# Optimization experiments

Measured on AMD Instinct MI355X. Metric: run time of the kernel, lower is better.

## Reference

```python
import jax, jax.numpy as jnp
import numpy as np

N_QUBITS = 10
DEPTH = 4
BATCH = 2048


def _ry(state, theta, q, n):
    # RY(theta) = [[cos(t/2), -sin(t/2)], [sin(t/2), cos(t/2)]], per-sample theta [B]
    B = state.shape[0]
    st = state.reshape(B, 2 ** q, 2, 2 ** (n - q - 1))
    c = jnp.cos(theta * 0.5)[:, None, None]
    s = jnp.sin(theta * 0.5)[:, None, None]
    a0, a1 = st[:, :, 0], st[:, :, 1]
    out = jnp.stack([c * a0 - s * a1, s * a0 + c * a1], axis=2)
    return out.reshape(B, -1)


def _rx(state, theta, q, n):
    # RX(theta) = [[cos(t/2), -i sin(t/2)], [-i sin(t/2), cos(t/2)]], shared scalar theta
    B = state.shape[0]
    st = state.reshape(B, 2 ** q, 2, 2 ** (n - q - 1))
    c = jnp.cos(theta * 0.5)
    s = jnp.sin(theta * 0.5)
    a0, a1 = st[:, :, 0], st[:, :, 1]
    out = jnp.stack([c * a0 - 1j * s * a1, -1j * s * a0 + c * a1], axis=2)
    return out.reshape(B, -1)


def _cnot(state, ctrl, tgt, n):
    # flip target amplitudes in the control=1 subspace
    B = state.shape[0]
    lo, hi = min(ctrl, tgt), max(ctrl, tgt)
    st = state.reshape(B, 2 ** lo, 2, 2 ** (hi - lo - 1), 2, 2 ** (n - hi - 1))
    if ctrl == lo:
        s0 = st[:, :, 0]                      # [B, 2^lo, mid, 2, rest]
        s1 = jnp.flip(st[:, :, 1], axis=3)    # flip target (axis 3 after indexing)
        out = jnp.stack([s0, s1], axis=2)
    else:
        s0 = st[:, :, :, :, 0]                # [B, 2^lo, 2, mid, rest]
        s1 = jnp.flip(st[:, :, :, :, 1], axis=2)  # flip target (axis 2)
        out = jnp.stack([s0, s1], axis=4)
    return out.reshape(B, -1)


def _circuit(x, w):
    B, n = x.shape
    depth = w.shape[0]
    state = jnp.zeros((B, 2 ** n), dtype=jnp.complex64).at[:, 0].set(1.0)
    # AngleEmbedding with RY rotations, per-sample angles
    for q in range(n):
        state = _ry(state, x[:, q], q, n)
    # BasicEntanglerLayers: RX on every wire, then CNOT ring
    for l in range(depth):
        for q in range(n):
            state = _rx(state, w[l, q], q, n)
        if n == 2:
            state = _cnot(state, 0, 1, n)
        else:
            for q in range(n):
                state = _cnot(state, q, (q + 1) % n, n)
    probs = state.real ** 2 + state.imag ** 2  # [B, 2^n]
    zs = []
    for q in range(n):
        m = probs.reshape(B, 2 ** q, 2, -1).sum(axis=(1, 3))  # marginal over wire q
        zs.append(m[:, 0] - m[:, 1])
    return jnp.stack(zs, axis=1)  # [B, n]


def setup_inputs() -> dict:
    key = jax.random.key(0)
    kx, kw = jax.random.split(key)
    x = jax.random.normal(kx, (BATCH, N_QUBITS), dtype=jnp.float32)
    q_weights = 0.02 * jax.random.normal(kw, (DEPTH, N_QUBITS), dtype=jnp.float32)
    return {"x": x, "q_weights": q_weights}


def reference(x, q_weights):
    return _circuit(x, q_weights)
```

## Files before the change

kernel.cpp:

```cpp
#include <hip/hip_runtime.h>

#define NQ 10
#define NR 16


__device__ __forceinline__ float xf(int i) { return __int_as_float(i); }
__device__ __forceinline__ int   fx(float f) { return __float_as_int(f); }

template<int M>
__device__ __forceinline__ float lane_xor(float v, int a32) {
    if constexpr (M == 1)
        return xf(__builtin_amdgcn_update_dpp(fx(v), fx(v), 0xB1, 0xF, 0xF, true));
    else if constexpr (M == 2)
        return xf(__builtin_amdgcn_update_dpp(fx(v), fx(v), 0x4E, 0xF, 0xF, true));
    else if constexpr (M == 8)
        return xf(__builtin_amdgcn_update_dpp(fx(v), fx(v), 0x128, 0xF, 0xF, true));
    else if constexpr (M == 4)
        return xf(__builtin_amdgcn_ds_swizzle(fx(v), 0x101F));
    else if constexpr (M == 16)
        return xf(__builtin_amdgcn_ds_swizzle(fx(v), 0x401F));
    else
        return xf(__builtin_amdgcn_ds_bpermute(a32, fx(v)));
}

__global__ __launch_bounds__(256, 2) void vql_kernel(
    const float* __restrict__ x,
    const float* __restrict__ w,
    float* __restrict__ out)
{
    const int lane = threadIdx.x & 63;
    const int b = blockIdx.x * 4 + (threadIdx.x >> 6);
    const int a32 = (lane ^ 32) << 2;

    const float2* xr = reinterpret_cast<const float2*>(x + b * NQ);
    const float2 x01 = xr[0], x23 = xr[1], x45 = xr[2], x67 = xr[3], x89 = xr[4];
    const float xa[NQ] = {0.5f * x01.x, 0.5f * x01.y, 0.5f * x23.x, 0.5f * x23.y,
                          0.5f * x45.x, 0.5f * x45.y, 0.5f * x67.x, 0.5f * x67.y,
                          0.5f * x89.x, 0.5f * x89.y};

    float F0r[NQ], F0i[NQ], F1r[NQ], F1i[NQ];
    #pragma unroll
    for (int q = 0; q < NQ; ++q) {
        float sy, cy, s, c;
        __sincosf(xa[q], &sy, &cy);
        __sincosf(0.5f * w[q], &s, &c);
        const float v0r = c * cy,  v0i = -s * sy;
        const float v1r = c * sy,  v1i = -s * cy;
        F0r[q] = v0r + v1r;  F0i[q] = v0i + v1i;
        F1r[q] = v0r - v1r;  F1i[q] = v0i - v1i;
    }

    const int L0 = lane & 1,        L1 = (lane >> 1) & 1, L2 = (lane >> 2) & 1;
    const int L3 = (lane >> 3) & 1, L4 = (lane >> 4) & 1, L5 = (lane >> 5) & 1;
    const int PL1 = L0 ^ L1, PL2 = PL1 ^ L2, PL3 = PL2 ^ L3, PL4 = PL3 ^ L4;
    const int g[7] = {PL4, PL4 ^ L5, PL3 ^ L5, PL2 ^ L5, PL1 ^ L5, L0 ^ L5, L5};
    #define SR_(q,bit) ((bit) ? F1r[q] : F0r[q])
    #define SI_(q,bit) ((bit) ? F1i[q] : F0i[q])

    float A_r[2], A_i[2];
    #pragma unroll
    for (int t = 0; t < 2; ++t) {
        float ar = SR_(0, g[0] ^ t), ai = SI_(0, g[0] ^ t);
        #pragma unroll
        for (int q = 1; q < 7; ++q) {
            const float br = SR_(q, g[q] ^ t), bi = SI_(q, g[q] ^ t);
            const float nr = ar * br - ai * bi;
            const float ni = ar * bi + ai * br;
            ar = nr; ai = ni;
        }
        A_r[t] = ar * (1.0f / 1024.0f);
        A_i[t] = ai * (1.0f / 1024.0f);
    }
    float Gr[2][2], Gi[2][2];
    #pragma unroll
    for (int t2 = 0; t2 < 2; ++t2)
        #pragma unroll
        for (int t1 = 0; t1 < 2; ++t1) {
            const float ar = SR_(8, t2 ^ L5), ai = SI_(8, t2 ^ L5);
            const float br = SR_(9, t1 ^ L5), bi = SI_(9, t1 ^ L5);
            Gr[t2][t1] = ar * br - ai * bi;
            Gi[t2][t1] = ar * bi + ai * br;
        }
    float Br_[2][2][2], Bi_[2][2][2];
    #pragma unroll
    for (int t3 = 0; t3 < 2; ++t3)
        #pragma unroll
        for (int t2 = 0; t2 < 2; ++t2)
            #pragma unroll
            for (int t1 = 0; t1 < 2; ++t1) {
                const float ar = SR_(7, t3 ^ L5), ai = SI_(7, t3 ^ L5);
                Br_[t3][t2][t1] = ar * Gr[t2][t1] - ai * Gi[t2][t1];
                Bi_[t3][t2][t1] = ar * Gi[t2][t1] + ai * Gr[t2][t1];
            }
    float re[NR], im[NR];
    #pragma unroll
    for (int r = 0; r < NR; ++r) {
        const int r0 = r & 1, r1 = (r >> 1) & 1, r2 = (r >> 2) & 1, r3 = (r >> 3) & 1;
        const int p1 = r0, p2 = r0 ^ r1, p3 = p2 ^ r2, p4 = p3 ^ r3;
        const float br = Br_[p3][p2][p1], bi = Bi_[p3][p2][p1];
        re[r] = A_r[p4] * br - A_i[p4] * bi;
        im[r] = A_r[p4] * bi + A_i[p4] * br;
    }
    #undef SR_
    #undef SI_

    float h1[NQ], h2[NQ], h3[NQ];
    #pragma unroll
    for (int q = 0; q < NQ; ++q) {
        h1[q] = 0.5f * w[NQ + q];
        h2[q] = 0.5f * w[2 * NQ + q];
        h3[q] = 0.5f * w[3 * NQ + q];
    }
    #define SG_(M) ((__builtin_popcount(lane & (M)) & 1) ? -1.f : 1.f)
    const float s1 = SG_(1),  s2 = SG_(2),  s3 = SG_(3),  s4 = SG_(4),  s5 = SG_(5);
    const float s6 = SG_(6),  s8 = SG_(8),  s10 = SG_(10), s12 = SG_(12);
    const float s16 = SG_(16), s20 = SG_(20), s24 = SG_(24), s32 = SG_(32);
    const float s40 = SG_(40), s48 = SG_(48);
    #undef SG_

    float C[NR];
    C[0]  = s32 * h1[0] + s16 * h1[1] + s8 * h1[2] + s4 * h1[3] + s2 * h1[4] + s1 * h1[5]
          + s48 * h2[0] + s24 * h2[1] + s12 * h2[2] + s6 * h2[3] + s3 * h2[4]
          + s40 * h3[0] + s20 * h3[1] + s10 * h3[2] + s5 * h3[3];
    C[8]  = h1[6] + s1 * h2[5] + s2 * h3[4];
    C[4]  = h1[7] + s1 * h3[5];
    C[2]  = h1[8] + s48 * h3[8];
    C[1]  = h1[9] + s48 * h2[9] + s24 * h3[9];
    C[12] = h2[6];
    C[6]  = h2[7];
    C[3]  = h2[8];
    C[10] = h3[6];
    C[5]  = h3[7];
    C[7] = 0.f; C[9] = 0.f; C[11] = 0.f; C[13] = 0.f; C[14] = 0.f; C[15] = 0.f;

    #pragma unroll
    for (int bset = 0; bset < 4; ++bset) {
        const int bb = 1 << bset;
        #pragma unroll
        for (int r = 0; r < NR; ++r) {
            if (!(r & bb)) {
                const float u = C[r], v = C[r | bb];
                C[r] = u + v;  C[r | bb] = u - v;
            }
        }
    }
    #pragma unroll
    for (int r = 0; r < NR; ++r) {
        float sp, cp;
        __sincosf(C[r], &sp, &cp);
        const float nr = re[r] * cp + im[r] * sp;
        const float ni = im[r] * cp - re[r] * sp;
        re[r] = nr; im[r] = ni;
    }

    #pragma unroll
    for (int bset = 0; bset < 4; ++bset) {
        const int bb = 1 << bset;
        #pragma unroll
        for (int r = 0; r < NR; ++r) {
            if (!(r & bb)) {
                float u = re[r], v = re[r | bb];
                re[r] = u + v;  re[r | bb] = u - v;
                u = im[r]; v = im[r | bb];
                im[r] = u + v;  im[r | bb] = u - v;
            }
        }
    }
    {
        const float sgA = (lane &  1) ? -1.f : 1.f;
        const float sgB = (lane &  2) ? -1.f : 1.f;
        const float sgC = (lane &  4) ? -1.f : 1.f;
        const float sgD = (lane &  8) ? -1.f : 1.f;
        const float sgE = (lane & 16) ? -1.f : 1.f;
        const float sgF = (lane & 32) ? -1.f : 1.f;
        #pragma unroll
        for (int r = 0; r < NR; ++r) {
            float p;
            p = lane_xor< 1>(re[r], a32); re[r] = fmaf(sgA, re[r], p);
            p = lane_xor< 1>(im[r], a32); im[r] = fmaf(sgA, im[r], p);
            p = lane_xor< 2>(re[r], a32); re[r] = fmaf(sgB, re[r], p);
            p = lane_xor< 2>(im[r], a32); im[r] = fmaf(sgB, im[r], p);
            p = lane_xor< 4>(re[r], a32); re[r] = fmaf(sgC, re[r], p);
            p = lane_xor< 4>(im[r], a32); im[r] = fmaf(sgC, im[r], p);
            p = lane_xor< 8>(re[r], a32); re[r] = fmaf(sgD, re[r], p);
            p = lane_xor< 8>(im[r], a32); im[r] = fmaf(sgD, im[r], p);
            p = lane_xor<16>(re[r], a32); re[r] = fmaf(sgE, re[r], p);
            p = lane_xor<16>(im[r], a32); im[r] = fmaf(sgE, im[r], p);
            p = lane_xor<32>(re[r], a32); re[r] = fmaf(sgF, re[r], p);
            p = lane_xor<32>(im[r], a32); im[r] = fmaf(sgF, im[r], p);
        }
    }

    float W[NR];
    #pragma unroll
    for (int r = 0; r < NR; ++r) W[r] = re[r] * re[r] + im[r] * im[r];
    #pragma unroll
    for (int bset = 0; bset < 4; ++bset) {
        const int bb = 1 << bset;
        #pragma unroll
        for (int r = 0; r < NR; ++r) {
            if (!(r & bb)) {
                const float u = W[r], v = W[r | bb];
                W[r] = u + v;  W[r | bb] = u - v;
            }
        }
    }
    const float sg44 = (__builtin_popcount(lane & 44) & 1) ? -1.f : 1.f;
    const float sg26 = (__builtin_popcount(lane & 26) & 1) ? -1.f : 1.f;
    const float sg13 = (__builtin_popcount(lane & 13) & 1) ? -1.f : 1.f;
    const float sg38 = (__builtin_popcount(lane & 38) & 1) ? -1.f : 1.f;
    const float sg51 = (__builtin_popcount(lane & 51) & 1) ? -1.f : 1.f;
    const float sg25 = (__builtin_popcount(lane & 25) & 1) ? -1.f : 1.f;
    const float sg12 = (__builtin_popcount(lane & 12) & 1) ? -1.f : 1.f;

    float z[NQ];
    z[0] = sg44 * W[12];
    z[1] = sg26 * W[10];
    z[2] = sg13 * W[ 5];
    z[3] = sg38 * W[10];
    z[4] = sg51 * W[ 5];
    z[5] = sg25 * W[10];
    z[6] = sg12 * W[13];
    z[7] = sg38 * W[ 6];
    z[8] = sg51 * W[ 3];
    z[9] = sg25 * W[ 9];

    #pragma unroll
    for (int q = 0; q < NQ; ++q) {
        z[q] += lane_xor<1>(z[q], a32);
        z[q] += lane_xor<2>(z[q], a32);
        z[q] += lane_xor<4>(z[q], a32);
        z[q] += lane_xor<8>(z[q], a32);
        z[q] += lane_xor<16>(z[q], a32);
        z[q] += lane_xor<32>(z[q], a32);
    }
    if (lane == 0) {
        float2* op = reinterpret_cast<float2*>(out + b * NQ);
        op[0] = make_float2(z[0], z[1]);
        op[1] = make_float2(z[2], z[3]);
        op[2] = make_float2(z[4], z[5]);
        op[3] = make_float2(z[6], z[7]);
        op[4] = make_float2(z[8], z[9]);
    }
}

extern "C" void kernel_launch(void* const* d_in, const int* in_sizes, int n_in,
                              void* d_out, int out_size, void* d_ws, size_t ws_size,
                              hipStream_t stream) {
    const float* x = (const float*)d_in[0];
    const float* w = (const float*)d_in[1];
    float* out = (float*)d_out;
    const int B = in_sizes[0] / NQ;
    vql_kernel<<<B / 4, 256, 0, stream>>>(x, w, out);
}
```

Measured before the change: 11.05 us.

## Compute Z expectations via correlation with permuted Fourier state instead of inverse transform

```diff
diff --git a/kernel.cpp b/kernel.cpp
--- a/kernel.cpp
+++ b/kernel.cpp
@@ -68,8 +68,8 @@
             const float ni = ar * bi + ai * br;
             ar = nr; ai = ni;
         }
-        A_r[t] = ar * (1.0f / 1024.0f);
-        A_i[t] = ai * (1.0f / 1024.0f);
+        A_r[t] = ar * (1.0f / 32.0f);
+        A_i[t] = ai * (1.0f / 32.0f);
     }
     float Gr[2][2], Gi[2][2];
     #pragma unroll
@@ -153,77 +153,122 @@
         re[r] = nr; im[r] = ni;
     }
 
-    #pragma unroll
-    for (int bset = 0; bset < 4; ++bset) {
-        const int bb = 1 << bset;
-        #pragma unroll
-        for (int r = 0; r < NR; ++r) {
-            if (!(r & bb)) {
-                float u = re[r], v = re[r | bb];
-                re[r] = u + v;  re[r | bb] = u - v;
-                u = im[r]; v = im[r | bb];
-                im[r] = u + v;  im[r | bb] = u - v;
-            }
-        }
-    }
-    {
-        const float sgA = (lane &  1) ? -1.f : 1.f;
-        const float sgB = (lane &  2) ? -1.f : 1.f;
-        const float sgC = (lane &  4) ? -1.f : 1.f;
-        const float sgD = (lane &  8) ? -1.f : 1.f;
-        const float sgE = (lane & 16) ? -1.f : 1.f;
-        const float sgF = (lane & 32) ? -1.f : 1.f;
-        #pragma unroll
-        for (int r = 0; r < NR; ++r) {
-            float p;
-            p = lane_xor< 1>(re[r], a32); re[r] = fmaf(sgA, re[r], p);
-            p = lane_xor< 1>(im[r], a32); im[r] = fmaf(sgA, im[r], p);
-            p = lane_xor< 2>(re[r], a32); re[r] = fmaf(sgB, re[r], p);
-            p = lane_xor< 2>(im[r], a32); im[r] = fmaf(sgB, im[r], p);
-            p = lane_xor< 4>(re[r], a32); re[r] = fmaf(sgC, re[r], p);
-            p = lane_xor< 4>(im[r], a32); im[r] = fmaf(sgC, im[r], p);
-            p = lane_xor< 8>(re[r], a32); re[r] = fmaf(sgD, re[r], p);
-            p = lane_xor< 8>(im[r], a32); im[r] = fmaf(sgD, im[r], p);
-            p = lane_xor<16>(re[r], a32); re[r] = fmaf(sgE, re[r], p);
-            p = lane_xor<16>(im[r], a32); im[r] = fmaf(sgE, im[r], p);
-            p = lane_xor<32>(re[r], a32); re[r] = fmaf(sgF, re[r], p);
-            p = lane_xor<32>(im[r], a32); im[r] = fmaf(sgF, im[r], p);
-        }
-    }
-
-    float W[NR];
-    #pragma unroll
-    for (int r = 0; r < NR; ++r) W[r] = re[r] * re[r] + im[r] * im[r];
-    #pragma unroll
-    for (int bset = 0; bset < 4; ++bset) {
-        const int bb = 1 << bset;
-        #pragma unroll
-        for (int r = 0; r < NR; ++r) {
-            if (!(r & bb)) {
-                const float u = W[r], v = W[r | bb];
-                W[r] = u + v;  W[r | bb] = u - v;
-            }
-        }
-    }
-    const float sg44 = (__builtin_popcount(lane & 44) & 1) ? -1.f : 1.f;
-    const float sg26 = (__builtin_popcount(lane & 26) & 1) ? -1.f : 1.f;
-    const float sg13 = (__builtin_popcount(lane & 13) & 1) ? -1.f : 1.f;
-    const float sg38 = (__builtin_popcount(lane & 38) & 1) ? -1.f : 1.f;
-    const float sg51 = (__builtin_popcount(lane & 51) & 1) ? -1.f : 1.f;
-    const float sg25 = (__builtin_popcount(lane & 25) & 1) ? -1.f : 1.f;
-    const float sg12 = (__builtin_popcount(lane & 12) & 1) ? -1.f : 1.f;
-
+    const int a44 = (lane ^ 44) << 2;
+    const int a38 = (lane ^ 38) << 2;
+    const int a51 = (lane ^ 51) << 2;
     float z[NQ];
-    z[0] = sg44 * W[12];
-    z[1] = sg26 * W[10];
-    z[2] = sg13 * W[ 5];
-    z[3] = sg38 * W[10];
-    z[4] = sg51 * W[ 5];
-    z[5] = sg25 * W[10];
-    z[6] = sg12 * W[13];
-    z[7] = sg38 * W[ 6];
-    z[8] = sg51 * W[ 3];
-    z[9] = sg25 * W[ 9];
+
+    {
+        float sr[NR], si[NR];
+        #pragma unroll
+        for (int r = 0; r < NR; ++r) {
+            sr[r] = xf(__builtin_amdgcn_ds_bpermute(a44, fx(re[r])));
+            si[r] = xf(__builtin_amdgcn_ds_bpermute(a44, fx(im[r])));
+        }
+        float ar_ = 0.f, ai_ = 0.f;
+        #pragma unroll
+        for (int r = 0; r < NR; ++r) {
+            ar_ = fmaf(re[r], sr[r ^ 12], ar_);
+            ai_ = fmaf(im[r], si[r ^ 12], ai_);
+        }
+        z[0] = ar_ + ai_;
+    }
+    {
+        float sr[NR], si[NR];
+        #pragma unroll
+        for (int r = 0; r < NR; ++r) {
+            sr[r] = xf(__builtin_amdgcn_ds_swizzle(fx(re[r]), 0x681F));
+            si[r] = xf(__builtin_amdgcn_ds_swizzle(fx(im[r]), 0x681F));
+        }
+        float ar_ = 0.f, ai_ = 0.f;
+        #pragma unroll
+        for (int r = 0; r < NR; ++r) {
+            ar_ = fmaf(re[r], sr[r ^ 10], ar_);
+            ai_ = fmaf(im[r], si[r ^ 10], ai_);
+        }
+        z[1] = ar_ + ai_;
+    }
+    {
+        float sr[NR], si[NR];
+        #pragma unroll
+        for (int r = 0; r < NR; ++r) {
+            sr[r] = xf(__builtin_amdgcn_ds_swizzle(fx(re[r]), 0x341F));
+            si[r] = xf(__builtin_amdgcn_ds_swizzle(fx(im[r]), 0x341F));
+        }
+        float ar_ = 0.f, ai_ = 0.f;
+        #pragma unroll
+        for (int r = 0; r < NR; ++r) {
+            ar_ = fmaf(re[r], sr[r ^ 5], ar_);
+            ai_ = fmaf(im[r], si[r ^ 5], ai_);
+        }
+        z[2] = ar_ + ai_;
+    }
+    {
+        float sr[NR], si[NR];
+        #pragma unroll
+        for (int r = 0; r < NR; ++r) {
+            sr[r] = xf(__builtin_amdgcn_ds_bpermute(a38, fx(re[r])));
+            si[r] = xf(__builtin_amdgcn_ds_bpermute(a38, fx(im[r])));
+        }
+        float a3r = 0.f, a3i = 0.f, a7r = 0.f, a7i = 0.f;
+        #pragma unroll
+        for (int r = 0; r < NR; ++r) {
+            a3r = fmaf(re[r], sr[r ^ 10], a3r);
+            a3i = fmaf(im[r], si[r ^ 10], a3i);
+            a7r = fmaf(re[r], sr[r ^ 6], a7r);
+            a7i = fmaf(im[r], si[r ^ 6], a7i);
+        }
+        z[3] = a3r + a3i;  z[7] = a7r + a7i;
+    }
+    {
+        float sr[NR], si[NR];
+        #pragma unroll
+        for (int r = 0; r < NR; ++r) {
+            sr[r] = xf(__builtin_amdgcn_ds_bpermute(a51, fx(re[r])));
+            si[r] = xf(__builtin_amdgcn_ds_bpermute(a51, fx(im[r])));
+        }
+        float a4r = 0.f, a4i = 0.f, a8r = 0.f, a8i = 0.f;
+        #pragma unroll
+        for (int r = 0; r < NR; ++r) {
+            a4r = fmaf(re[r], sr[r ^ 5], a4r);
+            a4i = fmaf(im[r], si[r ^ 5], a4i);
+            a8r = fmaf(re[r], sr[r ^ 3], a8r);
+            a8i = fmaf(im[r], si[r ^ 3], a8i);
+        }
+        z[4] = a4r + a4i;  z[8] = a8r + a8i;
+    }
+    {
+        float sr[NR], si[NR];
+        #pragma unroll
+        for (int r = 0; r < NR; ++r) {
+            sr[r] = xf(__builtin_amdgcn_ds_swizzle(fx(re[r]), 0x641F));
+            si[r] = xf(__builtin_amdgcn_ds_swizzle(fx(im[r]), 0x641F));
+        }
+        float a5r = 0.f, a5i = 0.f, a9r = 0.f, a9i = 0.f;
+        #pragma unroll
+        for (int r = 0; r < NR; ++r) {
+            a5r = fmaf(re[r], sr[r ^ 10], a5r);
+            a5i = fmaf(im[r], si[r ^ 10], a5i);
+            a9r = fmaf(re[r], sr[r ^ 9], a9r);
+            a9i = fmaf(im[r], si[r ^ 9], a9i);
+        }
+        z[5] = a5r + a5i;  z[9] = a9r + a9i;
+    }
+    {
+        float sr[NR], si[NR];
+        #pragma unroll
+        for (int r = 0; r < NR; ++r) {
+            sr[r] = xf(__builtin_amdgcn_ds_swizzle(fx(re[r]), 0x301F));
+            si[r] = xf(__builtin_amdgcn_ds_swizzle(fx(im[r]), 0x301F));
+        }
+        float ar_ = 0.f, ai_ = 0.f;
+        #pragma unroll
+        for (int r = 0; r < NR; ++r) {
+            ar_ = fmaf(re[r], sr[r ^ 13], ar_);
+            ai_ = fmaf(im[r], si[r ^ 13], ai_);
+        }
+        z[6] = ar_ + ai_;
+    }
 
     #pragma unroll
     for (int q = 0; q < NQ; ++q) {
```

Result: slower. 11.92 us (+7.8%).
